# Kernel optimization log

Measured on AMD Instinct MI355X. Metric: run time of the kernel, lower is better.

Reference implementation:

```python
import jax, jax.numpy as jnp
import numpy as np

N = 8192
D = 128
LMBD = 0.1
SPARSITY = 0.99  # fraction of zero entries in A


def setup_inputs() -> dict:
    key = jax.random.key(0)
    kA, kW = jax.random.split(key)
    u = jax.random.uniform(kA, (N, N), dtype=jnp.float32)
    A = jnp.where(u > SPARSITY, u, 0.0)
    W = jax.random.normal(kW, (N, D), dtype=jnp.float32) * 0.02
    b = jnp.zeros((D,), dtype=jnp.float32)
    return {"A": A, "W": W, "b": b}


def reference(A, W, b):
    # model(tf.eye(N)) with Dense(d) == eye(N) @ W + b == W + b  -> [N, d]
    Y = W + b
    # main loss: 0.5 * sum(mask * (A - Y Y^T)^2), mask = (A > 0)
    R = A - jnp.matmul(Y, Y.T)  # [N, N]
    main_loss = 0.5 * jnp.sum(jnp.where(A > 0, R * R, 0.0))
    # reg loss: lmbd/2 * ||Y||_F^2
    reg_loss = 0.5 * LMBD * jnp.sum(Y * Y)
    return main_loss + reg_loss
```

## Files before the change

kernel.cpp:

```cpp
#include <hip/hip_runtime.h>

#define N 8192
#define D 128
#define MAXNZ 256

typedef float nt_float4 __attribute__((ext_vector_type(4)));

__device__ __forceinline__ float wave_reduce(float p) {
    #pragma unroll
    for (int off = 32; off > 0; off >>= 1)
        p += __shfl_xor(p, off, 64);
    return p;
}

__global__ __launch_bounds__(256, 6)
void gf_main_kernel(const float* __restrict__ A,
                    const float* __restrict__ W,
                    const float* __restrict__ b,
                    float* __restrict__ partials) {
    __shared__ int   s_col[4][MAXNZ];
    __shared__ float s_val[4][MAXNZ];
    __shared__ float s_bsum[4];

    const int lane = threadIdx.x & 63;
    const int w    = threadIdx.x >> 6;
    const int row  = blockIdx.x * 4 + w;

    const float2 bb = ((const float2*)b)[lane];
    float2 yi = ((const float2*)(W + (size_t)row * D))[lane];
    yi.x += bb.x; yi.y += bb.y;

    const nt_float4* Arow = (const nt_float4*)(A + (size_t)row * N);
    const unsigned long long lmask = (1ull << lane) - 1ull;

    nt_float4 pf[4];
    #pragma unroll
    for (int k = 0; k < 4; ++k) pf[k] = __builtin_nontemporal_load(&Arow[k * 64 + lane]);

    int cnt = 0;
    for (int it = 0; it < 8; ++it) {
        nt_float4 cur[4];
        #pragma unroll
        for (int k = 0; k < 4; ++k) cur[k] = pf[k];
        if (it < 7) {
            #pragma unroll
            for (int k = 0; k < 4; ++k)
                pf[k] = __builtin_nontemporal_load(&Arow[(it + 1) * 256 + k * 64 + lane]);
        }
        #pragma unroll
        for (int k = 0; k < 4; ++k) {
            const int base_col = (it * 4 + k) * 256 + lane * 4;
            const float av4[4] = {cur[k].x, cur[k].y, cur[k].z, cur[k].w};
            #pragma unroll
            for (int q = 0; q < 4; ++q) {
                const unsigned long long m = __ballot(av4[q] > 0.0f);
                if (av4[q] > 0.0f) {
                    const int pos = cnt + __popcll(m & lmask);
                    if (pos < MAXNZ) {
                        s_col[w][pos] = base_col + q;
                        s_val[w][pos] = av4[q];
                    }
                }
                cnt += __popcll(m);
            }
        }
    }
    if (cnt > MAXNZ) cnt = MAXNZ;
    __syncthreads();

    float acc = 0.0f;
    float2 yjn[4];
    float  avn[4];
    #pragma unroll
    for (int k = 0; k < 4; ++k) {
        const bool valid = k < cnt;
        const int  idx   = valid ? k : 0;
        const int  j     = s_col[w][idx];
        avn[k]           = valid ? s_val[w][idx] : 0.0f;
        yjn[k]           = ((const float2*)(W + (size_t)j * D))[lane];
    }

    for (int t = 0; t < cnt; t += 4) {
        float2 yj[4];
        float  av[4];
        #pragma unroll
        for (int k = 0; k < 4; ++k) { yj[k] = yjn[k]; av[k] = avn[k]; }

        if (t + 4 < cnt) {
            #pragma unroll
            for (int k = 0; k < 4; ++k) {
                const bool valid = (t + 4 + k) < cnt;
                const int  idx   = valid ? (t + 4 + k) : 0;
                const int  j     = s_col[w][idx];
                avn[k]           = valid ? s_val[w][idx] : 0.0f;
                yjn[k]           = ((const float2*)(W + (size_t)j * D))[lane];
            }
        }

        float p[4];
        #pragma unroll
        for (int k = 0; k < 4; ++k)
            p[k] = yi.x * (yj[k].x + bb.x) + yi.y * (yj[k].y + bb.y);

        #pragma unroll
        for (int off = 32; off > 0; off >>= 1) {
            #pragma unroll
            for (int k = 0; k < 4; ++k)
                p[k] += __shfl_xor(p[k], off, 64);
        }

        #pragma unroll
        for (int k = 0; k < 4; ++k) {
            if ((t + k) < cnt) {
                const float r = av[k] - p[k];
                acc += r * r;
            }
        }
    }

    const float reg = wave_reduce(yi.x * yi.x + yi.y * yi.y);
    const float total = 0.5f * acc + 0.05f * reg;
    if (lane == 0) s_bsum[w] = total;
    __syncthreads();
    if (threadIdx.x == 0)
        partials[blockIdx.x] = s_bsum[0] + s_bsum[1] + s_bsum[2] + s_bsum[3];
}

__global__ __launch_bounds__(256)
void gf_reduce_kernel(const float* __restrict__ partials, float* __restrict__ out) {
    __shared__ float s_ws[4];
    const int lane = threadIdx.x & 63;
    const int w    = threadIdx.x >> 6;
    float s = 0.0f;
    for (int i = threadIdx.x; i < N / 4; i += 256) s += partials[i];
    s = wave_reduce(s);
    if (lane == 0) s_ws[w] = s;
    __syncthreads();
    if (threadIdx.x == 0) out[0] = s_ws[0] + s_ws[1] + s_ws[2] + s_ws[3];
}

extern "C" void kernel_launch(void* const* d_in, const int* in_sizes, int n_in,
                              void* d_out, int out_size, void* d_ws, size_t ws_size,
                              hipStream_t stream) {
    const float* A = (const float*)d_in[0];
    const float* W = (const float*)d_in[1];
    const float* b = (const float*)d_in[2];
    float* out = (float*)d_out;
    float* partials = (float*)d_ws;

    gf_main_kernel<<<dim3(N / 4), dim3(256), 0, stream>>>(A, W, b, partials);
    gf_reduce_kernel<<<dim3(1), dim3(256), 0, stream>>>(partials, out);
}
```

Baseline: 378.8 us.

## Split sparse residual into compaction pass and load-balanced global dot pass

The single fused kernel is split in two. A streaming kernel scans A, writes Y = W + b, and compacts the nonzeros into a global COO buffer using an atomic counter. A separate grid-stride kernel then computes each nonzero's dot product with 16 lanes per entry and software-prefetches the next entries. This is meant to separate the bandwidth-bound scan from the latency-bound gathers and balance the gather work across the whole GPU. In exchange it adds a global buffer write and read-back, plus two extra launches (init and dot), and relies on the workspace being large enough (about 20 MB).

```diff
diff --git a/kernel.cpp b/kernel.cpp
--- a/kernel.cpp
+++ b/kernel.cpp
@@ -3,8 +3,14 @@
 #define N 8192
 #define D 128
 #define MAXNZ 256
+#define NZCAP (1 << 20)
 
 typedef float nt_float4 __attribute__((ext_vector_type(4)));
+
+#define Y_OFF     0
+#define NZ_OFF    (4u * 1024 * 1024)
+#define PART_OFF  (20u * 1024 * 1024)
+#define GCNT_OFF  (PART_OFF + 4096u * 4)
 
 __device__ __forceinline__ float wave_reduce(float p) {
     #pragma unroll
@@ -13,11 +19,16 @@
     return p;
 }
 
+__global__ void gf_init_kernel(int* gcnt) { *gcnt = 0; }
+
 __global__ __launch_bounds__(256, 6)
-void gf_main_kernel(const float* __restrict__ A,
-                    const float* __restrict__ W,
-                    const float* __restrict__ b,
-                    float* __restrict__ partials) {
+void gf_stream_kernel(const float* __restrict__ A,
+                      const float* __restrict__ W,
+                      const float* __restrict__ b,
+                      float* __restrict__ Y,
+                      int4* __restrict__ nzbuf,
+                      float* __restrict__ partials,
+                      int* __restrict__ gcnt) {
     __shared__ int   s_col[4][MAXNZ];
     __shared__ float s_val[4][MAXNZ];
     __shared__ float s_bsum[4];
@@ -29,6 +40,7 @@
     const float2 bb = ((const float2*)b)[lane];
     float2 yi = ((const float2*)(W + (size_t)row * D))[lane];
     yi.x += bb.x; yi.y += bb.y;
+    ((float2*)(Y + (size_t)row * D))[lane] = yi;
 
     const nt_float4* Arow = (const nt_float4*)(A + (size_t)row * N);
     const unsigned long long lmask = (1ull << lane) - 1ull;
@@ -66,64 +78,81 @@
         }
     }
     if (cnt > MAXNZ) cnt = MAXNZ;
-    __syncthreads();
 
-    float acc = 0.0f;
-    float2 yjn[4];
-    float  avn[4];
-    #pragma unroll
-    for (int k = 0; k < 4; ++k) {
-        const bool valid = k < cnt;
-        const int  idx   = valid ? k : 0;
-        const int  j     = s_col[w][idx];
-        avn[k]           = valid ? s_val[w][idx] : 0.0f;
-        yjn[k]           = ((const float2*)(W + (size_t)j * D))[lane];
-    }
-
-    for (int t = 0; t < cnt; t += 4) {
-        float2 yj[4];
-        float  av[4];
-        #pragma unroll
-        for (int k = 0; k < 4; ++k) { yj[k] = yjn[k]; av[k] = avn[k]; }
-
-        if (t + 4 < cnt) {
-            #pragma unroll
-            for (int k = 0; k < 4; ++k) {
-                const bool valid = (t + 4 + k) < cnt;
-                const int  idx   = valid ? (t + 4 + k) : 0;
-                const int  j     = s_col[w][idx];
-                avn[k]           = valid ? s_val[w][idx] : 0.0f;
-                yjn[k]           = ((const float2*)(W + (size_t)j * D))[lane];
-            }
-        }
-
-        float p[4];
-        #pragma unroll
-        for (int k = 0; k < 4; ++k)
-            p[k] = yi.x * (yj[k].x + bb.x) + yi.y * (yj[k].y + bb.y);
-
-        #pragma unroll
-        for (int off = 32; off > 0; off >>= 1) {
-            #pragma unroll
-            for (int k = 0; k < 4; ++k)
-                p[k] += __shfl_xor(p[k], off, 64);
-        }
-
-        #pragma unroll
-        for (int k = 0; k < 4; ++k) {
-            if ((t + k) < cnt) {
-                const float r = av[k] - p[k];
-                acc += r * r;
-            }
-        }
-    }
+    int base = 0;
+    if (lane == 0) base = atomicAdd(gcnt, cnt);
+    base = __shfl(base, 0, 64);
+    if (base + cnt > NZCAP) cnt = NZCAP - base;
+    for (int t = lane; t < cnt; t += 64)
+        nzbuf[base + t] = make_int4(row, s_col[w][t], __float_as_int(s_val[w][t]), 0);
 
     const float reg = wave_reduce(yi.x * yi.x + yi.y * yi.y);
-    const float total = 0.5f * acc + 0.05f * reg;
-    if (lane == 0) s_bsum[w] = total;
+    if (lane == 0) s_bsum[w] = 0.05f * reg;
     __syncthreads();
     if (threadIdx.x == 0)
         partials[blockIdx.x] = s_bsum[0] + s_bsum[1] + s_bsum[2] + s_bsum[3];
+}
+
+__global__ __launch_bounds__(256, 6)
+void gf_dot_kernel(const float* __restrict__ Y,
+                   const int4* __restrict__ nzbuf,
+                   const int* __restrict__ gcnt,
+                   float* __restrict__ partials) {
+    __shared__ float s_bsum[4];
+    const int lane = threadIdx.x & 63;
+    const int w    = threadIdx.x >> 6;
+    const int s    = lane & 15;
+
+    const int total  = min(*gcnt, NZCAP);
+    const int stride = gridDim.x * 16;
+    const int qid    = blockIdx.x * 16 + w * 4 + (lane >> 4);
+
+    float acc = 0.0f;
+    int4 nzA, nzB;
+    float4 yiA0, yiA1, yjA0, yjA1;
+    {
+        const int iA = (qid < total) ? qid : 0;
+        nzA = nzbuf[iA];
+        const int iB = (qid + stride < total) ? (qid + stride) : 0;
+        nzB = nzbuf[iB];
+        const float* Yi = Y + (size_t)(nzA.x & (N - 1)) * D;
+        const float* Yj = Y + (size_t)(nzA.y & (N - 1)) * D;
+        yiA0 = ((const float4*)Yi)[s * 2]; yiA1 = ((const float4*)Yi)[s * 2 + 1];
+        yjA0 = ((const float4*)Yj)[s * 2]; yjA1 = ((const float4*)Yj)[s * 2 + 1];
+    }
+
+    for (int t = qid; t < total; t += stride) {
+        float4 yiB0, yiB1, yjB0, yjB1;
+        {
+            const float* Yi = Y + (size_t)(nzB.x & (N - 1)) * D;
+            const float* Yj = Y + (size_t)(nzB.y & (N - 1)) * D;
+            yiB0 = ((const float4*)Yi)[s * 2]; yiB1 = ((const float4*)Yi)[s * 2 + 1];
+            yjB0 = ((const float4*)Yj)[s * 2]; yjB1 = ((const float4*)Yj)[s * 2 + 1];
+        }
+        int4 nzC;
+        {
+            const int iC = (t + 2 * stride < total) ? (t + 2 * stride) : 0;
+            nzC = nzbuf[iC];
+        }
+        float p = yiA0.x * yjA0.x + yiA0.y * yjA0.y + yiA0.z * yjA0.z + yiA0.w * yjA0.w
+                + yiA1.x * yjA1.x + yiA1.y * yjA1.y + yiA1.z * yjA1.z + yiA1.w * yjA1.w;
+        #pragma unroll
+        for (int off = 8; off > 0; off >>= 1)
+            p += __shfl_xor(p, off, 64);
+        if (s == 0) {
+            const float r = __int_as_float(nzA.z) - p;
+            acc += r * r;
+        }
+        nzA = nzB; nzB = nzC;
+        yiA0 = yiB0; yiA1 = yiB1; yjA0 = yjB0; yjA1 = yjB1;
+    }
+
+    acc = wave_reduce(acc);
+    if (lane == 0) s_bsum[w] = acc;
+    __syncthreads();
+    if (threadIdx.x == 0)
+        partials[2048 + blockIdx.x] =
+            0.5f * (s_bsum[0] + s_bsum[1] + s_bsum[2] + s_bsum[3]);
 }
 
 __global__ __launch_bounds__(256)
@@ -132,7 +161,7 @@
     const int lane = threadIdx.x & 63;
     const int w    = threadIdx.x >> 6;
     float s = 0.0f;
-    for (int i = threadIdx.x; i < N / 4; i += 256) s += partials[i];
+    for (int i = threadIdx.x; i < 4096; i += 256) s += partials[i];
     s = wave_reduce(s);
     if (lane == 0) s_ws[w] = s;
     __syncthreads();
@@ -146,8 +175,15 @@
     const float* W = (const float*)d_in[1];
     const float* b = (const float*)d_in[2];
     float* out = (float*)d_out;
-    float* partials = (float*)d_ws;
 
-    gf_main_kernel<<<dim3(N / 4), dim3(256), 0, stream>>>(A, W, b, partials);
+    char* ws = (char*)d_ws;
+    float* Y        = (float*)(ws + Y_OFF);
+    int4*  nzbuf    = (int4*)(ws + NZ_OFF);
+    float* partials = (float*)(ws + PART_OFF);
+    int*   gcnt     = (int*)(ws + GCNT_OFF);
+
+    gf_init_kernel<<<dim3(1), dim3(1), 0, stream>>>(gcnt);
+    gf_stream_kernel<<<dim3(N / 4), dim3(256), 0, stream>>>(A, W, b, Y, nzbuf, partials, gcnt);
+    gf_dot_kernel<<<dim3(2048), dim3(256), 0, stream>>>(Y, nzbuf, gcnt, partials);
     gf_reduce_kernel<<<dim3(1), dim3(256), 0, stream>>>(partials, out);
 }
```

Result: slower. 442.4 us (+16.8%).

## Split wave into four 16-lane groups each computing one nonzero's dot product

Applied to the files above, without the earlier changes.

The gather phase now assigns each 16-lane quarter of the wavefront its own nonzero column. Each lane loads two float4 chunks of the neighbour's W row, and a 4-step shuffle reduction replaces the 6-step full-wave reduction over four values. The bias term is folded algebraically into a precomputed yi·b scalar, and loads are software-pipelined two iterations ahead. This cuts cross-lane shuffle work and uses wider loads, at the cost of more registers per lane and partial-lane accumulation.

```diff
diff --git a/kernel.cpp b/kernel.cpp
--- a/kernel.cpp
+++ b/kernel.cpp
@@ -25,10 +25,19 @@
     const int lane = threadIdx.x & 63;
     const int w    = threadIdx.x >> 6;
     const int row  = blockIdx.x * 4 + w;
+    const int q    = lane >> 4;
+    const int s    = lane & 15;
 
-    const float2 bb = ((const float2*)b)[lane];
-    float2 yi = ((const float2*)(W + (size_t)row * D))[lane];
-    yi.x += bb.x; yi.y += bb.y;
+    const float4* B4   = (const float4*)b;
+    const float4  b0   = B4[s * 2];
+    const float4  b1   = B4[s * 2 + 1];
+    const float4* Wrow = (const float4*)(W + (size_t)row * D);
+    float4 yi0 = Wrow[s * 2];
+    float4 yi1 = Wrow[s * 2 + 1];
+    yi0.x += b0.x; yi0.y += b0.y; yi0.z += b0.z; yi0.w += b0.w;
+    yi1.x += b1.x; yi1.y += b1.y; yi1.z += b1.z; yi1.w += b1.w;
+    const float yib = yi0.x * b0.x + yi0.y * b0.y + yi0.z * b0.z + yi0.w * b0.w
+                    + yi1.x * b1.x + yi1.y * b1.y + yi1.z * b1.z + yi1.w * b1.w;
 
     const nt_float4* Arow = (const nt_float4*)(A + (size_t)row * N);
     const unsigned long long lmask = (1ull << lane) - 1ull;
@@ -52,13 +61,13 @@
             const int base_col = (it * 4 + k) * 256 + lane * 4;
             const float av4[4] = {cur[k].x, cur[k].y, cur[k].z, cur[k].w};
             #pragma unroll
-            for (int q = 0; q < 4; ++q) {
-                const unsigned long long m = __ballot(av4[q] > 0.0f);
-                if (av4[q] > 0.0f) {
+            for (int p = 0; p < 4; ++p) {
+                const unsigned long long m = __ballot(av4[p] > 0.0f);
+                if (av4[p] > 0.0f) {
                     const int pos = cnt + __popcll(m & lmask);
                     if (pos < MAXNZ) {
-                        s_col[w][pos] = base_col + q;
-                        s_val[w][pos] = av4[q];
+                        s_col[w][pos] = base_col + p;
+                        s_val[w][pos] = av4[p];
                     }
                 }
                 cnt += __popcll(m);
@@ -69,57 +78,53 @@
     __syncthreads();
 
     float acc = 0.0f;
-    float2 yjn[4];
-    float  avn[4];
-    #pragma unroll
-    for (int k = 0; k < 4; ++k) {
-        const bool valid = k < cnt;
-        const int  idx   = valid ? k : 0;
-        const int  j     = s_col[w][idx];
-        avn[k]           = valid ? s_val[w][idx] : 0.0f;
-        yjn[k]           = ((const float2*)(W + (size_t)j * D))[lane];
+    int   jn;  float avc, avn;
+    float4 ga0, ga1;
+    {
+        const int i0 = (q < cnt) ? q : 0;
+        const int j0 = s_col[w][i0] & (N - 1);
+        avc = (q < cnt) ? s_val[w][i0] : 0.0f;
+        const float4* Yj = (const float4*)(W + (size_t)j0 * D);
+        ga0 = Yj[s * 2]; ga1 = Yj[s * 2 + 1];
+    }
+    {
+        const int t1 = 4 + q;
+        const int i1 = (t1 < cnt) ? t1 : 0;
+        jn  = s_col[w][i1] & (N - 1);
+        avn = (t1 < cnt) ? s_val[w][i1] : 0.0f;
     }
 
     for (int t = 0; t < cnt; t += 4) {
-        float2 yj[4];
-        float  av[4];
+        const float4 yj0 = ga0, yj1 = ga1;
+        const float  ava = avc;
+        {
+            const float4* Yj = (const float4*)(W + (size_t)jn * D);
+            ga0 = Yj[s * 2]; ga1 = Yj[s * 2 + 1];
+        }
+        {
+            const int t2 = t + 8 + q;
+            const int i2 = (t2 < cnt) ? t2 : 0;
+            jn  = s_col[w][i2] & (N - 1);
+            avc = avn;
+            avn = (t2 < cnt) ? s_val[w][i2] : 0.0f;
+        }
+        float p = yi0.x * yj0.x + yi0.y * yj0.y + yi0.z * yj0.z + yi0.w * yj0.w
+                + yi1.x * yj1.x + yi1.y * yj1.y + yi1.z * yj1.z + yi1.w * yj1.w
+                + yib;
         #pragma unroll
-        for (int k = 0; k < 4; ++k) { yj[k] = yjn[k]; av[k] = avn[k]; }
-
-        if (t + 4 < cnt) {
-            #pragma unroll
-            for (int k = 0; k < 4; ++k) {
-                const bool valid = (t + 4 + k) < cnt;
-                const int  idx   = valid ? (t + 4 + k) : 0;
-                const int  j     = s_col[w][idx];
-                avn[k]           = valid ? s_val[w][idx] : 0.0f;
-                yjn[k]           = ((const float2*)(W + (size_t)j * D))[lane];
-            }
-        }
-
-        float p[4];
-        #pragma unroll
-        for (int k = 0; k < 4; ++k)
-            p[k] = yi.x * (yj[k].x + bb.x) + yi.y * (yj[k].y + bb.y);
-
-        #pragma unroll
-        for (int off = 32; off > 0; off >>= 1) {
-            #pragma unroll
-            for (int k = 0; k < 4; ++k)
-                p[k] += __shfl_xor(p[k], off, 64);
-        }
-
-        #pragma unroll
-        for (int k = 0; k < 4; ++k) {
-            if ((t + k) < cnt) {
-                const float r = av[k] - p[k];
-                acc += r * r;
-            }
+        for (int off = 8; off > 0; off >>= 1)
+            p += __shfl_xor(p, off, 64);
+        if (s == 0 && (t + q) < cnt) {
+            const float r = ava - p;
+            acc += r * r;
         }
     }
 
-    const float reg = wave_reduce(yi.x * yi.x + yi.y * yi.y);
-    const float total = 0.5f * acc + 0.05f * reg;
+    float regp = 0.0f;
+    if (q == 0)
+        regp = yi0.x * yi0.x + yi0.y * yi0.y + yi0.z * yi0.z + yi0.w * yi0.w
+             + yi1.x * yi1.x + yi1.y * yi1.y + yi1.z * yi1.z + yi1.w * yi1.w;
+    const float total = wave_reduce(0.5f * acc + 0.05f * regp);
     if (lane == 0) s_bsum[w] = total;
     __syncthreads();
     if (threadIdx.x == 0)
```

Result: faster. 353.6 us (-6.7%).
